# Optimization experiments

Measured on AMD Instinct MI355X. Metric: run time of the kernel, lower is better.

## Reference

```python
import jax, jax.numpy as jnp
import numpy as np


def setup_inputs() -> dict:
    key = jax.random.key(0)
    ks = jax.random.split(key, 7)
    B, T, D, H, C = 256, 512, 128, 512, 10
    s_ih = 1.0 / np.sqrt(H)
    return {
        "X": jax.random.normal(ks[0], (B, T, D), dtype=jnp.float32),
        "W_ih": jax.random.normal(ks[1], (4 * H, D), dtype=jnp.float32) * s_ih,
        "W_hh": jax.random.normal(ks[2], (4 * H, H), dtype=jnp.float32) * s_ih,
        "b_ih": jax.random.normal(ks[3], (4 * H,), dtype=jnp.float32) * s_ih,
        "b_hh": jax.random.normal(ks[4], (4 * H,), dtype=jnp.float32) * s_ih,
        "W_lin": jax.random.normal(ks[5], (C, H), dtype=jnp.float32) * s_ih,
        "b_lin": jax.random.normal(ks[6], (C,), dtype=jnp.float32) * s_ih,
    }


def _lstm_mean_h(X, W_ih, W_hh, b_ih, b_hh):
    B, T, D = X.shape
    H = W_hh.shape[1]
    # Input projections for all timesteps at once: [T, B, 4H]
    x_proj = jnp.einsum("btd,kd->tbk", X, W_ih) + b_ih + b_hh

    def step(carry, xp):
        h, c = carry
        gates = xp + h @ W_hh.T  # [B, 4H]
        i, f, g, o = jnp.split(gates, 4, axis=-1)  # PyTorch i,f,g,o order
        i = jax.nn.sigmoid(i)
        f = jax.nn.sigmoid(f)
        g = jnp.tanh(g)
        o = jax.nn.sigmoid(o)
        c = f * c + i * g
        h = o * jnp.tanh(c)
        return (h, c), h

    h0 = jnp.zeros((B, H), dtype=X.dtype)
    (_, _), hs = jax.lax.scan(step, (h0, h0), x_proj)  # hs: [T, B, H]
    return jnp.mean(hs, axis=0)  # == sum(h_t)/T


def reference(X, W_ih, W_hh, b_ih, b_hh, W_lin, b_lin):
    states = _lstm_mean_h(X, W_ih, W_hh, b_ih, b_hh)  # [B, H]
    logits = states @ W_lin.T + b_lin  # [B, num_classes]
    return logits
```

## Files before the change

kernel.cpp:

```cpp
#include <hip/hip_runtime.h>
#include <stdint.h>


#define T_STEPS 512
#define BATCH   256
#define DIM     128
#define HID     512
#define NGRP    16
#define BT      16
#define RBUF    4

typedef _Float16 half8 __attribute__((ext_vector_type(8)));
typedef _Float16 half4 __attribute__((ext_vector_type(4)));
typedef float    f32x4 __attribute__((ext_vector_type(4)));
typedef unsigned u32x4 __attribute__((ext_vector_type(4)));

#define SLOT_HALFS (BATCH * HID)
#define SLOT_U64   (SLOT_HALFS / 4)
#define FLG_OFF    (RBUF * SLOT_HALFS * 2)
#define WS_NEEDED  (FLG_OFF + NGRP * 32 * 128)

__device__ __forceinline__ half8 cvt8(f32x4 a, f32x4 b) {
  half8 r;
  r[0]=(_Float16)a[0]; r[1]=(_Float16)a[1]; r[2]=(_Float16)a[2]; r[3]=(_Float16)a[3];
  r[4]=(_Float16)b[0]; r[5]=(_Float16)b[1]; r[6]=(_Float16)b[2]; r[7]=(_Float16)b[3];
  return r;
}
__device__ __forceinline__ half8 load8_cvt(const float* p) {
  const f32x4* q = (const f32x4*)p;
  return cvt8(q[0], q[1]);
}
__device__ __forceinline__ float fsig(float x) {
  return __builtin_amdgcn_rcpf(1.f + __expf(-x));
}
__device__ __forceinline__ float ftanh(float x) {
  return 1.f - 2.f * __builtin_amdgcn_rcpf(1.f + __expf(2.f * x));
}

union h4u { unsigned long long u; half4 h; };
union c16 { unsigned long long u2[2]; u32x4 v; };

__global__ __launch_bounds__(256, 1) void lstm_persistent(
    const float* __restrict__ X,   const float* __restrict__ Wih,
    const float* __restrict__ Whh, const float* __restrict__ bih,
    const float* __restrict__ bhh, const float* __restrict__ Wlin,
    float* __restrict__ out, _Float16* __restrict__ hbuf,
    unsigned* __restrict__ flg)
{
  __shared__ unsigned hsh[2][4096];

  const int tid  = threadIdx.x;
  const int w    = tid >> 6;
  const int lane = tid & 63;
  const int col  = lane & 15;
  const int q    = lane >> 4;
  const int bid  = blockIdx.x;
  const int g    = bid & 15;
  const int blk  = bid >> 4;
  const int J    = blk * 64 + w * 16;
  const int wid  = blk * 4 + w;
  const int b_my = g * BT + col;

  half8 whh[16][4];
  half8 wih[4][4];
  #pragma unroll
  for (int kc = 0; kc < 16; ++kc)
    #pragma unroll
    for (int mt = 0; mt < 4; ++mt) {
      const int row = mt * HID + J + col;
      whh[kc][mt] = load8_cvt(Whh + (size_t)row * HID + kc * 32 + q * 8);
    }
  #pragma unroll
  for (int xc = 0; xc < 4; ++xc)
    #pragma unroll
    for (int mt = 0; mt < 4; ++mt) {
      const int row = mt * HID + J + col;
      wih[xc][mt] = load8_cvt(Wih + (size_t)row * DIM + xc * 32 + q * 8);
    }

  float bias[4][4], c_st[4], hsum[4];
  #pragma unroll
  for (int mt = 0; mt < 4; ++mt)
    #pragma unroll
    for (int r = 0; r < 4; ++r) {
      const int row = mt * HID + J + q * 4 + r;
      bias[mt][r] = bih[row] + bhh[row];
    }
  #pragma unroll
  for (int r = 0; r < 4; ++r) { c_st[r] = 0.f; hsum[r] = 0.f; }

  unsigned* gflg = flg + (size_t)g * 32 * 32;
  const float* Xb = X + (size_t)b_my * T_STEPS * DIM;
  unsigned long long* h64 = (unsigned long long*)hbuf;
  const size_t pub_u64 = ((size_t)b_my * HID + J + q * 4) >> 2;
  const size_t con_u64 = ((size_t)b_my * HID) >> 2;

  const int  pw   = 8 * w + (lane & 7);
  const bool self = (pw == wid);
  unsigned* pollp = gflg + (size_t)pw * 32;

  f32x4 xr0[8], xr1[8];
  #pragma unroll
  for (int xc = 0; xc < 4; ++xc) {
    const f32x4* p = (const f32x4*)(Xb + xc * 32 + q * 8);
    xr0[2 * xc] = p[0]; xr0[2 * xc + 1] = p[1];
  }
  f32x4 acc[4];
  #pragma unroll
  for (int mt = 0; mt < 4; ++mt) acc[mt] = (f32x4){0.f, 0.f, 0.f, 0.f};
  #pragma unroll
  for (int xc = 0; xc < 4; ++xc) {
    half8 xb = cvt8(xr0[2 * xc], xr0[2 * xc + 1]);
    #pragma unroll
    for (int mt = 0; mt < 4; ++mt)
      acc[mt] = __builtin_amdgcn_mfma_f32_16x16x32_f16(wih[xc][mt], xb, acc[mt], 0, 0, 0);
  }
  #pragma unroll
  for (int xc = 0; xc < 4; ++xc) {
    const f32x4* p1 = (const f32x4*)(Xb + (size_t)1 * DIM + xc * 32 + q * 8);
    const f32x4* p2 = (const f32x4*)(Xb + (size_t)2 * DIM + xc * 32 + q * 8);
    xr1[2 * xc] = p1[0]; xr1[2 * xc + 1] = p1[1];
    xr0[2 * xc] = p2[0]; xr0[2 * xc + 1] = p2[1];
  }

  for (int t = 0; t < T_STEPS; ++t) {
    if (t > 0) {
      for (;;) {
        unsigned v = __hip_atomic_load(pollp, __ATOMIC_RELAXED,
                                       __HIP_MEMORY_SCOPE_AGENT);
        if (self) v = 0xFFFFFFFFu;
        if (__all((int)(v >= (unsigned)t))) break;
      }
      __builtin_amdgcn_sched_barrier(0);

      unsigned long long lo[4], hi[4];
      {
        const unsigned long long* base =
            h64 + (size_t)(t & 3) * SLOT_U64 + con_u64;
        #pragma unroll
        for (int i = 0; i < 4; ++i) {
          const int kc = w * 4 + i;
          lo[i] = __hip_atomic_load(base + kc * 8 + q * 2,     __ATOMIC_RELAXED, __HIP_MEMORY_SCOPE_AGENT);
          hi[i] = __hip_atomic_load(base + kc * 8 + q * 2 + 1, __ATOMIC_RELAXED, __HIP_MEMORY_SCOPE_AGENT);
        }
      }
      #pragma unroll
      for (int i = 0; i < 4; ++i) {
        const int kc = w * 4 + i;
        c16 u; u.u2[0] = lo[i]; u.u2[1] = hi[i];
        *(u32x4*)(&hsh[t & 1][kc * 256 + q * 64 + col * 4]) = u.v;
      }
      __syncthreads();

      #pragma unroll
      for (int kc = 0; kc < 16; ++kc) {
        const half8 hbv = *(const half8*)(&hsh[t & 1][kc * 256 + q * 64 + col * 4]);
        #pragma unroll
        for (int mt = 0; mt < 4; ++mt)
          acc[mt] = __builtin_amdgcn_mfma_f32_16x16x32_f16(whh[kc][mt], hbv, acc[mt], 0, 0, 0);
      }
    }

    h4u hv;
    #pragma unroll
    for (int r = 0; r < 4; ++r) {
      const float ig = fsig(acc[0][r] + bias[0][r]);
      const float fg = fsig(acc[1][r] + bias[1][r]);
      const float gg = ftanh(acc[2][r] + bias[2][r]);
      const float og = fsig(acc[3][r] + bias[3][r]);
      const float cc = fg * c_st[r] + ig * gg;
      c_st[r] = cc;
      const float h = og * ftanh(cc);
      hsum[r] += h;
      hv.h[r] = (_Float16)h;
    }

    if (t + 1 < T_STEPS) {
      __hip_atomic_store(h64 + (size_t)((t + 1) & 3) * SLOT_U64 + pub_u64,
                         hv.u, __ATOMIC_RELAXED, __HIP_MEMORY_SCOPE_AGENT);

      asm volatile("s_waitcnt vmcnt(0)" ::: "memory");
      if (lane == 0)
        __hip_atomic_store(gflg + (size_t)wid * 32, (unsigned)(t + 1),
                           __ATOMIC_RELAXED, __HIP_MEMORY_SCOPE_AGENT);

      {
        const int tn = (t + 2 < T_STEPS) ? (t + 2) : (T_STEPS - 1);
        const float* xp = Xb + (size_t)tn * DIM + q * 8;
        f32x4* dst = (t & 1) ? xr1 : xr0;
        #pragma unroll
        for (int xc = 0; xc < 4; ++xc) {
          const f32x4* src = (const f32x4*)(xp + xc * 32);
          dst[2 * xc]     = src[0];
          dst[2 * xc + 1] = src[1];
        }
      }

      #pragma unroll
      for (int mt = 0; mt < 4; ++mt) acc[mt] = (f32x4){0.f, 0.f, 0.f, 0.f};
      const f32x4* xbuf = ((t + 1) & 1) ? xr1 : xr0;
      #pragma unroll
      for (int xc = 0; xc < 4; ++xc) {
        half8 xb = cvt8(xbuf[2 * xc], xbuf[2 * xc + 1]);
        #pragma unroll
        for (int mt = 0; mt < 4; ++mt)
          acc[mt] = __builtin_amdgcn_mfma_f32_16x16x32_f16(wih[xc][mt], xb, acc[mt], 0, 0, 0);
      }
    }
  }

  const float inv = 1.0f / (float)T_STEPS;
  float m[4];
  #pragma unroll
  for (int r = 0; r < 4; ++r) m[r] = hsum[r] * inv;
  #pragma unroll
  for (int cls = 0; cls < 10; ++cls) {
    f32x4 wl = *(const f32x4*)(Wlin + (size_t)cls * HID + J + q * 4);
    float p = m[0] * wl[0] + m[1] * wl[1] + m[2] * wl[2] + m[3] * wl[3];
    p += __shfl_xor(p, 16, 64);
    p += __shfl_xor(p, 32, 64);
    if (q == 0) atomicAdd(out + b_my * 10 + cls, p);
  }
}

__global__ void init_out(const float* __restrict__ blin, float* __restrict__ out) {
  const int i = blockIdx.x * blockDim.x + threadIdx.x;
  if (i < BATCH * 10) out[i] = blin[i % 10];
}

extern "C" void kernel_launch(void* const* d_in, const int* in_sizes, int n_in,
                              void* d_out, int out_size, void* d_ws, size_t ws_size,
                              hipStream_t stream) {
  const float* X    = (const float*)d_in[0];
  const float* Wih  = (const float*)d_in[1];
  const float* Whh  = (const float*)d_in[2];
  const float* bih  = (const float*)d_in[3];
  const float* bhh  = (const float*)d_in[4];
  const float* Wlin = (const float*)d_in[5];
  const float* blin = (const float*)d_in[6];
  float* out = (float*)d_out;

  if (ws_size < (size_t)WS_NEEDED) return;

  _Float16* hbuf = (_Float16*)d_ws;
  unsigned* flg  = (unsigned*)((char*)d_ws + FLG_OFF);

  hipMemsetAsync((char*)d_ws + FLG_OFF, 0, NGRP * 32 * 128, stream);
  init_out<<<10, 256, 0, stream>>>(blin, out);
  lstm_persistent<<<128, 256, 0, stream>>>(X, Wih, Whh, bih, bhh, Wlin, out,
                                           hbuf, flg);
}
```

Before: 2.884 ms.

## Detect same-XCD group placement and use sc0 cache-local cross-block exchange

At kernel start the blocks run a handshake. Each block writes a magic word and polls its group peers' words with sc0 loads, which bypass only the local L1, and then all blocks in the group vote. If every peer's write is visible this way, the group is taken to share an L2, and the main loop switches to sc0 loads and plain volatile stores for the flag polling and the h exchange, in place of agent-scope atomics. This aims to cut the latency of the per-step cross-block synchronisation, at the cost of a startup handshake, a duplicated loop and reliance on block placement across XCDs.

```diff
diff --git a/kernel.cpp b/kernel.cpp
--- a/kernel.cpp
+++ b/kernel.cpp
@@ -9,6 +9,8 @@
 #define NGRP    16
 #define BT      16
 #define RBUF    4
+#define MAGIC   0x5EED5EEDu
+#define HSHAKE_BOUND 8192
 
 typedef _Float16 half8 __attribute__((ext_vector_type(8)));
 typedef _Float16 half4 __attribute__((ext_vector_type(4)));
@@ -18,7 +20,9 @@
 #define SLOT_HALFS (BATCH * HID)
 #define SLOT_U64   (SLOT_HALFS / 4)
 #define FLG_OFF    (RBUF * SLOT_HALFS * 2)
-#define WS_NEEDED  (FLG_OFF + NGRP * 32 * 128)
+#define TEST_OFF   (FLG_OFF + NGRP * 32 * 128)
+#define VOTE_OFF   (TEST_OFF + 128 * 128)
+#define WS_NEEDED  (VOTE_OFF + 128 * 128)
 
 __device__ __forceinline__ half8 cvt8(f32x4 a, f32x4 b) {
   half8 r;
@@ -36,6 +40,12 @@
 __device__ __forceinline__ float ftanh(float x) {
   return 1.f - 2.f * __builtin_amdgcn_rcpf(1.f + __expf(2.f * x));
 }
+__device__ __forceinline__ unsigned ld_sc0_u32(const unsigned* p) {
+  unsigned v;
+  asm volatile("global_load_dword %0, %1, off sc0\n\ts_waitcnt vmcnt(0)"
+               : "=v"(v) : "v"(p) : "memory");
+  return v;
+}
 
 union h4u { unsigned long long u; half4 h; };
 union c16 { unsigned long long u2[2]; u32x4 v; };
@@ -45,9 +55,11 @@
     const float* __restrict__ Whh, const float* __restrict__ bih,
     const float* __restrict__ bhh, const float* __restrict__ Wlin,
     float* __restrict__ out, _Float16* __restrict__ hbuf,
-    unsigned* __restrict__ flg)
+    unsigned* __restrict__ flg, unsigned* __restrict__ test,
+    unsigned* __restrict__ vote)
 {
   __shared__ unsigned hsh[2][4096];
+  __shared__ int s_mode;
 
   const int tid  = threadIdx.x;
   const int w    = tid >> 6;
@@ -89,6 +101,36 @@
   #pragma unroll
   for (int r = 0; r < 4; ++r) { c_st[r] = 0.f; hsum[r] = 0.f; }
 
+  if (w == 0) {
+    if (lane == 0) {
+      *(volatile unsigned*)(test + (size_t)bid * 32) = MAGIC;
+      asm volatile("s_waitcnt vmcnt(0)" ::: "memory");
+    }
+    int seen = 1;
+    if (lane < 8) {
+      const unsigned* tp = test + (size_t)(g + 16 * lane) * 32;
+      seen = 0;
+      for (int it = 0; it < HSHAKE_BOUND && !seen; ++it)
+        seen = (ld_sc0_u32(tp) == MAGIC);
+    }
+    int ok = __all(seen);
+    if (lane == 0)
+      __hip_atomic_store(vote + (size_t)bid * 32, ok ? 2u : 1u,
+                         __ATOMIC_RELAXED, __HIP_MEMORY_SCOPE_AGENT);
+    int vok = 1;
+    if (lane < 8) {
+      unsigned v;
+      do {
+        v = __hip_atomic_load(vote + (size_t)(g + 16 * lane) * 32,
+                              __ATOMIC_RELAXED, __HIP_MEMORY_SCOPE_AGENT);
+      } while (v == 0u);
+      vok = (v == 2u);
+    }
+    if (lane == 0) s_mode = __all(vok);
+  }
+  __syncthreads();
+  const int local = s_mode;
+
   unsigned* gflg = flg + (size_t)g * 32 * 32;
   const float* Xb = X + (size_t)b_my * T_STEPS * DIM;
   unsigned long long* h64 = (unsigned long long*)hbuf;
@@ -123,88 +165,183 @@
     xr0[2 * xc] = p2[0]; xr0[2 * xc + 1] = p2[1];
   }
 
-  for (int t = 0; t < T_STEPS; ++t) {
-    if (t > 0) {
-      for (;;) {
-        unsigned v = __hip_atomic_load(pollp, __ATOMIC_RELAXED,
-                                       __HIP_MEMORY_SCOPE_AGENT);
-        if (self) v = 0xFFFFFFFFu;
-        if (__all((int)(v >= (unsigned)t))) break;
-      }
-      __builtin_amdgcn_sched_barrier(0);
-
-      unsigned long long lo[4], hi[4];
-      {
-        const unsigned long long* base =
-            h64 + (size_t)(t & 3) * SLOT_U64 + con_u64;
+  if (local) {
+    for (int t = 0; t < T_STEPS; ++t) {
+      if (t > 0) {
+        for (;;) {
+          unsigned v = ld_sc0_u32(pollp);
+          if (self) v = 0xFFFFFFFFu;
+          if (__all((int)(v >= (unsigned)t))) break;
+        }
+        __builtin_amdgcn_sched_barrier(0);
+
+        unsigned long long L0,H0,L1,H1,L2x,H2,L3,H3;
+        {
+          const unsigned long long* base =
+              h64 + (size_t)(t & 3) * SLOT_U64 + con_u64 + q * 2;
+          const unsigned long long* b0 = base + (size_t)(4 * w + 0) * 8;
+          const unsigned long long* b1 = base + (size_t)(4 * w + 1) * 8;
+          const unsigned long long* b2 = base + (size_t)(4 * w + 2) * 8;
+          const unsigned long long* b3 = base + (size_t)(4 * w + 3) * 8;
+          asm volatile(
+            "global_load_dwordx2 %0, %8, off sc0\n\t"
+            "global_load_dwordx2 %1, %8, off offset:8 sc0\n\t"
+            "global_load_dwordx2 %2, %9, off sc0\n\t"
+            "global_load_dwordx2 %3, %9, off offset:8 sc0\n\t"
+            "global_load_dwordx2 %4, %10, off sc0\n\t"
+            "global_load_dwordx2 %5, %10, off offset:8 sc0\n\t"
+            "global_load_dwordx2 %6, %11, off sc0\n\t"
+            "global_load_dwordx2 %7, %11, off offset:8 sc0\n\t"
+            "s_waitcnt vmcnt(0)"
+            : "=&v"(L0), "=&v"(H0), "=&v"(L1), "=&v"(H1),
+              "=&v"(L2x), "=&v"(H2), "=&v"(L3), "=&v"(H3)
+            : "v"(b0), "v"(b1), "v"(b2), "v"(b3)
+            : "memory");
+        }
+        { c16 u; u.u2[0]=L0; u.u2[1]=H0;
+          *(u32x4*)(&hsh[t & 1][(4*w+0)*256 + q*64 + col*4]) = u.v; }
+        { c16 u; u.u2[0]=L1; u.u2[1]=H1;
+          *(u32x4*)(&hsh[t & 1][(4*w+1)*256 + q*64 + col*4]) = u.v; }
+        { c16 u; u.u2[0]=L2x; u.u2[1]=H2;
+          *(u32x4*)(&hsh[t & 1][(4*w+2)*256 + q*64 + col*4]) = u.v; }
+        { c16 u; u.u2[0]=L3; u.u2[1]=H3;
+          *(u32x4*)(&hsh[t & 1][(4*w+3)*256 + q*64 + col*4]) = u.v; }
+        __syncthreads();
+
+        #pragma unroll
+        for (int kc = 0; kc < 16; ++kc) {
+          const half8 hbv = *(const half8*)(&hsh[t & 1][kc * 256 + q * 64 + col * 4]);
+          #pragma unroll
+          for (int mt = 0; mt < 4; ++mt)
+            acc[mt] = __builtin_amdgcn_mfma_f32_16x16x32_f16(whh[kc][mt], hbv, acc[mt], 0, 0, 0);
+        }
+      }
+
+      h4u hv;
+      #pragma unroll
+      for (int r = 0; r < 4; ++r) {
+        const float ig = fsig(acc[0][r] + bias[0][r]);
+        const float fg = fsig(acc[1][r] + bias[1][r]);
+        const float gg = ftanh(acc[2][r] + bias[2][r]);
+        const float og = fsig(acc[3][r] + bias[3][r]);
+        const float cc = fg * c_st[r] + ig * gg;
+        c_st[r] = cc;
+        const float h = og * ftanh(cc);
+        hsum[r] += h;
+        hv.h[r] = (_Float16)h;
+      }
+
+      if (t + 1 < T_STEPS) {
+        *(volatile unsigned long long*)
+            (h64 + (size_t)((t + 1) & 3) * SLOT_U64 + pub_u64) = hv.u;
+        asm volatile("s_waitcnt vmcnt(0)" ::: "memory");
+        if (lane == 0)
+          *(volatile unsigned*)(gflg + (size_t)wid * 32) = (unsigned)(t + 1);
+
+        {
+          const int tn = (t + 2 < T_STEPS) ? (t + 2) : (T_STEPS - 1);
+          const float* xp = Xb + (size_t)tn * DIM + q * 8;
+          f32x4* dst = (t & 1) ? xr1 : xr0;
+          #pragma unroll
+          for (int xc = 0; xc < 4; ++xc) {
+            const f32x4* src = (const f32x4*)(xp + xc * 32);
+            dst[2 * xc]     = src[0];
+            dst[2 * xc + 1] = src[1];
+          }
+        }
+        #pragma unroll
+        for (int mt = 0; mt < 4; ++mt) acc[mt] = (f32x4){0.f, 0.f, 0.f, 0.f};
+        const f32x4* xbuf = ((t + 1) & 1) ? xr1 : xr0;
+        #pragma unroll
+        for (int xc = 0; xc < 4; ++xc) {
+          half8 xb = cvt8(xbuf[2 * xc], xbuf[2 * xc + 1]);
+          #pragma unroll
+          for (int mt = 0; mt < 4; ++mt)
+            acc[mt] = __builtin_amdgcn_mfma_f32_16x16x32_f16(wih[xc][mt], xb, acc[mt], 0, 0, 0);
+        }
+      }
+    }
+  } else {
+    for (int t = 0; t < T_STEPS; ++t) {
+      if (t > 0) {
+        for (;;) {
+          unsigned v = __hip_atomic_load(pollp, __ATOMIC_RELAXED,
+                                         __HIP_MEMORY_SCOPE_AGENT);
+          if (self) v = 0xFFFFFFFFu;
+          if (__all((int)(v >= (unsigned)t))) break;
+        }
+        __builtin_amdgcn_sched_barrier(0);
+
+        unsigned long long lo[4], hi[4];
+        {
+          const unsigned long long* base =
+              h64 + (size_t)(t & 3) * SLOT_U64 + con_u64;
+          #pragma unroll
+          for (int i = 0; i < 4; ++i) {
+            const int kc = w * 4 + i;
+            lo[i] = __hip_atomic_load(base + kc * 8 + q * 2,     __ATOMIC_RELAXED, __HIP_MEMORY_SCOPE_AGENT);
+            hi[i] = __hip_atomic_load(base + kc * 8 + q * 2 + 1, __ATOMIC_RELAXED, __HIP_MEMORY_SCOPE_AGENT);
+          }
+        }
         #pragma unroll
         for (int i = 0; i < 4; ++i) {
           const int kc = w * 4 + i;
-          lo[i] = __hip_atomic_load(base + kc * 8 + q * 2,     __ATOMIC_RELAXED, __HIP_MEMORY_SCOPE_AGENT);
-          hi[i] = __hip_atomic_load(base + kc * 8 + q * 2 + 1, __ATOMIC_RELAXED, __HIP_MEMORY_SCOPE_AGENT);
-        }
-      }
+          c16 u; u.u2[0] = lo[i]; u.u2[1] = hi[i];
+          *(u32x4*)(&hsh[t & 1][kc * 256 + q * 64 + col * 4]) = u.v;
+        }
+        __syncthreads();
+
+        #pragma unroll
+        for (int kc = 0; kc < 16; ++kc) {
+          const half8 hbv = *(const half8*)(&hsh[t & 1][kc * 256 + q * 64 + col * 4]);
+          #pragma unroll
+          for (int mt = 0; mt < 4; ++mt)
+            acc[mt] = __builtin_amdgcn_mfma_f32_16x16x32_f16(whh[kc][mt], hbv, acc[mt], 0, 0, 0);
+        }
+      }
+
+      h4u hv;
       #pragma unroll
-      for (int i = 0; i < 4; ++i) {
-        const int kc = w * 4 + i;
-        c16 u; u.u2[0] = lo[i]; u.u2[1] = hi[i];
-        *(u32x4*)(&hsh[t & 1][kc * 256 + q * 64 + col * 4]) = u.v;
-      }
-      __syncthreads();
-
-      #pragma unroll
-      for (int kc = 0; kc < 16; ++kc) {
-        const half8 hbv = *(const half8*)(&hsh[t & 1][kc * 256 + q * 64 + col * 4]);
-        #pragma unroll
-        for (int mt = 0; mt < 4; ++mt)
-          acc[mt] = __builtin_amdgcn_mfma_f32_16x16x32_f16(whh[kc][mt], hbv, acc[mt], 0, 0, 0);
-      }
-    }
-
-    h4u hv;
-    #pragma unroll
-    for (int r = 0; r < 4; ++r) {
-      const float ig = fsig(acc[0][r] + bias[0][r]);
-      const float fg = fsig(acc[1][r] + bias[1][r]);
-      const float gg = ftanh(acc[2][r] + bias[2][r]);
-      const float og = fsig(acc[3][r] + bias[3][r]);
-      const float cc = fg * c_st[r] + ig * gg;
-      c_st[r] = cc;
-      const float h = og * ftanh(cc);
-      hsum[r] += h;
-      hv.h[r] = (_Float16)h;
-    }
-
-    if (t + 1 < T_STEPS) {
-      __hip_atomic_store(h64 + (size_t)((t + 1) & 3) * SLOT_U64 + pub_u64,
-                         hv.u, __ATOMIC_RELAXED, __HIP_MEMORY_SCOPE_AGENT);
-
-      asm volatile("s_waitcnt vmcnt(0)" ::: "memory");
-      if (lane == 0)
-        __hip_atomic_store(gflg + (size_t)wid * 32, (unsigned)(t + 1),
-                           __ATOMIC_RELAXED, __HIP_MEMORY_SCOPE_AGENT);
-
-      {
-        const int tn = (t + 2 < T_STEPS) ? (t + 2) : (T_STEPS - 1);
-        const float* xp = Xb + (size_t)tn * DIM + q * 8;
-        f32x4* dst = (t & 1) ? xr1 : xr0;
+      for (int r = 0; r < 4; ++r) {
+        const float ig = fsig(acc[0][r] + bias[0][r]);
+        const float fg = fsig(acc[1][r] + bias[1][r]);
+        const float gg = ftanh(acc[2][r] + bias[2][r]);
+        const float og = fsig(acc[3][r] + bias[3][r]);
+        const float cc = fg * c_st[r] + ig * gg;
+        c_st[r] = cc;
+        const float h = og * ftanh(cc);
+        hsum[r] += h;
+        hv.h[r] = (_Float16)h;
+      }
+
+      if (t + 1 < T_STEPS) {
+        __hip_atomic_store(h64 + (size_t)((t + 1) & 3) * SLOT_U64 + pub_u64,
+                           hv.u, __ATOMIC_RELAXED, __HIP_MEMORY_SCOPE_AGENT);
+        asm volatile("s_waitcnt vmcnt(0)" ::: "memory");
+        if (lane == 0)
+          __hip_atomic_store(gflg + (size_t)wid * 32, (unsigned)(t + 1),
+                             __ATOMIC_RELAXED, __HIP_MEMORY_SCOPE_AGENT);
+        {
+          const int tn = (t + 2 < T_STEPS) ? (t + 2) : (T_STEPS - 1);
+          const float* xp = Xb + (size_t)tn * DIM + q * 8;
+          f32x4* dst = (t & 1) ? xr1 : xr0;
+          #pragma unroll
+          for (int xc = 0; xc < 4; ++xc) {
+            const f32x4* src = (const f32x4*)(xp + xc * 32);
+            dst[2 * xc]     = src[0];
+            dst[2 * xc + 1] = src[1];
+          }
+        }
+        #pragma unroll
+        for (int mt = 0; mt < 4; ++mt) acc[mt] = (f32x4){0.f, 0.f, 0.f, 0.f};
+        const f32x4* xbuf = ((t + 1) & 1) ? xr1 : xr0;
         #pragma unroll
         for (int xc = 0; xc < 4; ++xc) {
-          const f32x4* src = (const f32x4*)(xp + xc * 32);
-          dst[2 * xc]     = src[0];
-          dst[2 * xc + 1] = src[1];
-        }
-      }
-
-      #pragma unroll
-      for (int mt = 0; mt < 4; ++mt) acc[mt] = (f32x4){0.f, 0.f, 0.f, 0.f};
-      const f32x4* xbuf = ((t + 1) & 1) ? xr1 : xr0;
-      #pragma unroll
-      for (int xc = 0; xc < 4; ++xc) {
-        half8 xb = cvt8(xbuf[2 * xc], xbuf[2 * xc + 1]);
-        #pragma unroll
-        for (int mt = 0; mt < 4; ++mt)
-          acc[mt] = __builtin_amdgcn_mfma_f32_16x16x32_f16(wih[xc][mt], xb, acc[mt], 0, 0, 0);
+          half8 xb = cvt8(xbuf[2 * xc], xbuf[2 * xc + 1]);
+          #pragma unroll
+          for (int mt = 0; mt < 4; ++mt)
+            acc[mt] = __builtin_amdgcn_mfma_f32_16x16x32_f16(wih[xc][mt], xb, acc[mt], 0, 0, 0);
+        }
       }
     }
   }
@@ -242,11 +379,13 @@
 
   if (ws_size < (size_t)WS_NEEDED) return;
 
-  _Float16* hbuf = (_Float16*)d_ws;
-  unsigned* flg  = (unsigned*)((char*)d_ws + FLG_OFF);
-
-  hipMemsetAsync((char*)d_ws + FLG_OFF, 0, NGRP * 32 * 128, stream);
+  _Float16* hbuf  = (_Float16*)d_ws;
+  unsigned* flg   = (unsigned*)((char*)d_ws + FLG_OFF);
+  unsigned* test  = (unsigned*)((char*)d_ws + TEST_OFF);
+  unsigned* vote  = (unsigned*)((char*)d_ws + VOTE_OFF);
+
+  hipMemsetAsync((char*)d_ws + FLG_OFF, 0, WS_NEEDED - FLG_OFF, stream);
   init_out<<<10, 256, 0, stream>>>(blin, out);
   lstm_persistent<<<128, 256, 0, stream>>>(X, Wih, Whh, bih, bhh, Wlin, out,
-                                           hbuf, flg);
-}
+                                           hbuf, flg, test, vote);
+}
```

Result: slower. 4.506 ms (+56.2%).
